# Kernel optimization log

Hardware: AMD Instinct MI355X
Metric: run time of the kernel (lower is better)

Reference implementation:

```python
import jax, jax.numpy as jnp
import numpy as np

K = 3  # reassembly kernel size (hardcoded in module)
S = 2  # upsample scale (hardcoded)
PAD = K // 2


def _nearest_up2(t):
    # F.interpolate(scale_factor=2, mode='nearest') on NCHW
    return jnp.repeat(jnp.repeat(t, 2, axis=2), 2, axis=3)


def _patches3x3(t):
    # F.unfold(kernel=3, pad=1) -> [B, C, 9, H, W], k = ki*3 + kj (row-major)
    B, C, H, W = t.shape
    tp = jnp.pad(t, ((0, 0), (0, 0), (PAD, PAD), (PAD, PAD)))
    return jnp.stack([tp[:, :, i:i + H, j:j + W] for i in range(K) for j in range(K)], axis=2)


def setup_inputs() -> dict:
    key = jax.random.key(0)
    k1, k2 = jax.random.split(key)
    x = jax.random.normal(k1, (2, 256, 128, 128), dtype=jnp.float32)
    W_off = jax.random.normal(k2, (2, 1, 5, 5), dtype=jnp.float32) * 1e-3  # normal_init std=0.001
    b_off = jnp.zeros((2,), dtype=jnp.float32)
    return {"x": x, "W_off": W_off, "b_off": b_off}


def reference(x, W_off, b_off):
    B, C, H, W = x.shape
    H2, W2 = S * H, S * W

    mean = jnp.mean(x, axis=1, keepdims=True)  # [B,1,H,W]

    # offset = tanh(conv5x5(nearest_up2(mean))) / 4 -> [B,2,2H,2W]
    mean_up = _nearest_up2(mean)
    off = jax.lax.conv_general_dilated(mean_up, W_off, (1, 1), ((2, 2), (2, 2)))
    offset = jnp.tanh(off + b_off[None, :, None, None]) / 4.0

    # center buffer: pixel_shuffle of [1,8,1,1]; per 2x2 cell, channel 0 varies with j, channel 1 with i
    cell = jnp.array([[[-0.25, 0.25], [-0.25, 0.25]],
                      [[-0.25, -0.25], [0.25, 0.25]]], dtype=x.dtype)  # [2(ch),2(i),2(j)]
    center = jnp.broadcast_to(cell[:, None, :, None, :], (2, H, 2, W, 2)).reshape(2, H2, W2)

    shift = center[None] + offset  # [B,2,2H,2W]

    # neighbor grid: n0 (fast, width) = [-1,0,1]*3 ; n1 (slow, height) = repeat([-1,0,1],3)
    n0 = jnp.tile(jnp.array([-1.0, 0.0, 1.0], dtype=x.dtype), 3)        # [9]
    n1 = jnp.repeat(jnp.array([-1.0, 0.0, 1.0], dtype=x.dtype), 3)      # [9]
    d2 = (shift[:, 0:1] - n0[None, :, None, None]) ** 2 + \
         (shift[:, 1:2] - n1[None, :, None, None]) ** 2                 # [B,9,2H,2W]
    kernels = 1.0 / (d2 + 0.2)

    # grad gating from 3x3 neighborhood of mean
    pm = _patches3x3(mean)[:, 0]            # [B,9,H,W]
    grad = pm - mean                        # broadcast over k
    grad = 1.0 / (grad ** 2 + 1.0)
    logits = _nearest_up2(grad) * kernels   # [B,9,2H,2W]
    kernels = jax.nn.softmax(logits, axis=1)

    # CARAFE: out[b,c,2h+p,2w+q] = sum_k kernels[b,k,2h+p,2w+q] * patches[b,c,k,h,w]
    patches = _patches3x3(x)                        # [B,C,9,H,W]
    Kr = kernels.reshape(B, K * K, H, S, W, S)      # [B,9,H,2,W,2]
    out = jnp.einsum('bkhpwq,bckhw->bchpwq', Kr, patches).reshape(B, C, H2, W2)
    return out
```

## Files before the change

### kernel.cpp

```cpp
#include <hip/hip_runtime.h>
#include <math.h>

#define B 2
#define C 256
#define H 128
#define W 128
#define H2 256
#define W2 256
#define CPT 16
#define TW 16

__global__ __launch_bounds__(1024) void mean_kernel(const float* __restrict__ x,
                                                    float* __restrict__ mean) {
    int bh = blockIdx.x;
    int b = bh / H, h = bh % H;
    int tid = threadIdx.x;
    int g  = tid >> 5;
    int w4 = tid & 31;

    const float4* xb = (const float4*)x + (size_t)b * C * (H * W / 4)
                       + (size_t)h * (W / 4) + w4;
    const size_t cstride = H * W / 4;

    float4 acc = make_float4(0.f, 0.f, 0.f, 0.f);
    #pragma unroll
    for (int i = 0; i < C / 32; ++i) {
        float4 v = xb[(size_t)(g * (C / 32) + i) * cstride];
        acc.x += v.x; acc.y += v.y; acc.z += v.z; acc.w += v.w;
    }

    __shared__ float4 sm[1024];
    sm[tid] = acc;
    __syncthreads();
    for (int s = 16; s >= 1; s >>= 1) {
        if (g < s) {
            float4 o = sm[tid + s * 32];
            acc.x += o.x; acc.y += o.y; acc.z += o.z; acc.w += o.w;
            sm[tid] = acc;
        }
        __syncthreads();
    }
    if (g == 0) {
        const float inv = 1.0f / C;
        float4 m = make_float4(acc.x * inv, acc.y * inv, acc.z * inv, acc.w * inv);
        ((float4*)mean)[(size_t)bh * (W / 4) + w4] = m;
    }
}

__global__ __launch_bounds__(256) void weights_kernel(const float* __restrict__ mean,
                                                      const float* __restrict__ Woff,
                                                      const float* __restrict__ boff,
                                                      float* __restrict__ Kw) {
    __shared__ float sm[10][12];
    __shared__ float sW[50];
    __shared__ float sb[2];

    int b  = blockIdx.z;
    int x0 = blockIdx.x * TW;
    int y0 = blockIdx.y * TW;
    int h0 = y0 >> 1, w0 = x0 >> 1;
    int tid = threadIdx.x;

    if (tid < 100) {
        int lh = tid / 10, lw = tid % 10;
        int hh = h0 - 1 + lh, ww = w0 - 1 + lw;
        sm[lh][lw] = (hh >= 0 && hh < H && ww >= 0 && ww < W)
                         ? mean[(size_t)b * H * W + hh * W + ww] : 0.f;
    }
    if (tid >= 128 && tid < 178) sW[tid - 128] = Woff[tid - 128];
    if (tid >= 192 && tid < 194) sb[tid - 192] = boff[tid - 192];
    __syncthreads();

    int tx = tid & 15, ty = tid >> 4;
    int y = y0 + ty, x = x0 + tx;

    float off0 = 0.f, off1 = 0.f;
    #pragma unroll
    for (int u = 0; u < 5; ++u) {
        int lh = ((y + u - 2) >> 1) - (h0 - 1);
        #pragma unroll
        for (int v = 0; v < 5; ++v) {
            int lw = ((x + v - 2) >> 1) - (w0 - 1);
            float m = sm[lh][lw];
            off0 += m * sW[u * 5 + v];
            off1 += m * sW[25 + u * 5 + v];
        }
    }
    float s0 = tanhf(off0 + sb[0]) * 0.25f + ((x & 1) ? 0.25f : -0.25f);
    float s1 = tanhf(off1 + sb[1]) * 0.25f + ((y & 1) ? 0.25f : -0.25f);

    int lhc = (ty >> 1) + 1;
    int lwc = (tx >> 1) + 1;
    float mc = sm[lhc][lwc];

    float lg[9];
    float mx = -1e30f;
    #pragma unroll
    for (int k = 0; k < 9; ++k) {
        int di = k / 3 - 1, dj = k % 3 - 1;
        float pm = sm[lhc + di][lwc + dj];
        float g = pm - mc;
        float grad = 1.0f / (g * g + 1.0f);
        float d0 = s0 - (float)dj;
        float d1 = s1 - (float)di;
        float kern = 1.0f / (d0 * d0 + d1 * d1 + 0.2f);
        float l = grad * kern;
        lg[k] = l;
        mx = fmaxf(mx, l);
    }
    float sum = 0.f;
    #pragma unroll
    for (int k = 0; k < 9; ++k) { lg[k] = expf(lg[k] - mx); sum += lg[k]; }
    float inv = 1.0f / sum;

    float* o = Kw + (size_t)b * 9 * (H2 * W2) + (size_t)y * W2 + x;
    #pragma unroll
    for (int k = 0; k < 9; ++k) o[(size_t)k * (H2 * W2)] = lg[k] * inv;
}

__global__ __launch_bounds__(256) void carafe_kernel(const float* __restrict__ x,
                                                     const float* __restrict__ Kw,
                                                     float* __restrict__ out) {
    int idx = blockIdx.x * blockDim.x + threadIdx.x;
    int w2 = idx & 63;
    int h  = (idx >> 6) & (H - 1);
    int cg = (idx >> 13) & (C / CPT - 1);
    int b  = idx >> 17;

    int w  = w2 * 2;
    int y0 = 2 * h, x0 = 2 * w;

    const float* kb = Kw + (size_t)b * 9 * (H2 * W2) + (size_t)y0 * W2 + x0;
    float4 wk[2][9];
    #pragma unroll
    for (int k = 0; k < 9; ++k) {
        wk[0][k] = *(const float4*)(kb + (size_t)k * (H2 * W2));
        wk[1][k] = *(const float4*)(kb + (size_t)k * (H2 * W2) + W2);
    }

    int off[3][4]; bool val[3][4];
    #pragma unroll
    for (int r = 0; r < 3; ++r) {
        int hh = h - 1 + r;
        #pragma unroll
        for (int c = 0; c < 4; ++c) {
            int ww = w - 1 + c;
            val[r][c] = (hh >= 0) & (hh < H) & (ww >= 0) & (ww < W);
            off[r][c] = hh * W + ww;
        }
    }

    const float* xb = x   + (size_t)(b * C + cg * CPT) * (H * W);
    float*       ob = out + (size_t)(b * C + cg * CPT) * (H2 * W2)
                          + (size_t)y0 * W2 + x0;

    #pragma unroll 2
    for (int cc = 0; cc < CPT; ++cc) {
        float p[3][4];
        #pragma unroll
        for (int r = 0; r < 3; ++r)
            #pragma unroll
            for (int c = 0; c < 4; ++c)
                p[r][c] = val[r][c] ? xb[off[r][c]] : 0.f;

        #pragma unroll
        for (int pp = 0; pp < 2; ++pp) {
            float4 acc = make_float4(0.f, 0.f, 0.f, 0.f);
            #pragma unroll
            for (int k = 0; k < 9; ++k) {
                int ki = k / 3, kj = k % 3;
                float a  = p[ki][kj];
                float bb = p[ki][kj + 1];
                acc.x += wk[pp][k].x * a;
                acc.y += wk[pp][k].y * a;
                acc.z += wk[pp][k].z * bb;
                acc.w += wk[pp][k].w * bb;
            }
            *(float4*)(ob + (size_t)pp * W2) = acc;
        }
        xb += H * W;
        ob += H2 * W2;
    }
}

extern "C" void kernel_launch(void* const* d_in, const int* in_sizes, int n_in,
                              void* d_out, int out_size, void* d_ws, size_t ws_size,
                              hipStream_t stream) {
    const float* x    = (const float*)d_in[0];
    const float* Woff = (const float*)d_in[1];
    const float* boff = (const float*)d_in[2];
    float* out = (float*)d_out;

    float* mean = (float*)d_ws;
    float* Kw   = mean + (size_t)B * H * W;

    mean_kernel<<<B * H, 1024, 0, stream>>>(x, mean);

    dim3 wgrid(W2 / TW, H2 / TW, B);
    weights_kernel<<<wgrid, 256, 0, stream>>>(mean, Woff, boff, Kw);

    int mt = B * (C / CPT) * H * (W / 2);
    carafe_kernel<<<mt / 256, 256, 0, stream>>>(x, Kw, out);
}
```

Baseline: 175.3 us.

## Fuse reassembly-weight computation into CARAFE kernel via shared-memory weight tile

Merges the weights kernel and the CARAFE kernel into one launch. Each block computes the softmax reassembly weights for a 16x16 output tile into shared memory, then reuses them across all 256 channels. This removes the global write and re-read of the 9-plane weight tensor and one kernel launch. In exchange the grid shrinks to 512 blocks, each thread handles 32 channels, and each warp covers a narrow 8-pixel-wide tile. That lowers parallelism and makes global loads and stores less coalesced.

```diff
diff --git a/kernel.cpp b/kernel.cpp
--- a/kernel.cpp
+++ b/kernel.cpp
@@ -7,8 +7,6 @@
 #define W 128
 #define H2 256
 #define W2 256
-#define CPT 16
-#define TW 16
 
 __global__ __launch_bounds__(1024) void mean_kernel(const float* __restrict__ x,
                                                     float* __restrict__ mean) {
@@ -47,18 +45,19 @@
     }
 }
 
-__global__ __launch_bounds__(256) void weights_kernel(const float* __restrict__ mean,
-                                                      const float* __restrict__ Woff,
-                                                      const float* __restrict__ boff,
-                                                      float* __restrict__ Kw) {
+__global__ __launch_bounds__(256) void fused_kernel(const float* __restrict__ x,
+                                                    const float* __restrict__ mean,
+                                                    const float* __restrict__ Woff,
+                                                    const float* __restrict__ boff,
+                                                    float* __restrict__ out) {
     __shared__ float sm[10][12];
     __shared__ float sW[50];
     __shared__ float sb[2];
+    __shared__ float sw[9][16][16];
 
     int b  = blockIdx.z;
-    int x0 = blockIdx.x * TW;
-    int y0 = blockIdx.y * TW;
-    int h0 = y0 >> 1, w0 = x0 >> 1;
+    int h0 = blockIdx.y * 8;
+    int w0 = blockIdx.x * 8;
     int tid = threadIdx.x;
 
     if (tid < 100) {
@@ -71,97 +70,90 @@
     if (tid >= 192 && tid < 194) sb[tid - 192] = boff[tid - 192];
     __syncthreads();
 
-    int tx = tid & 15, ty = tid >> 4;
-    int y = y0 + ty, x = x0 + tx;
+    {
+        int tx = tid & 15, ty = tid >> 4;
 
-    float off0 = 0.f, off1 = 0.f;
-    #pragma unroll
-    for (int u = 0; u < 5; ++u) {
-        int lh = ((y + u - 2) >> 1) - (h0 - 1);
+        float off0 = 0.f, off1 = 0.f;
         #pragma unroll
-        for (int v = 0; v < 5; ++v) {
-            int lw = ((x + v - 2) >> 1) - (w0 - 1);
-            float m = sm[lh][lw];
-            off0 += m * sW[u * 5 + v];
-            off1 += m * sW[25 + u * 5 + v];
+        for (int u = 0; u < 5; ++u) {
+            int lh = ((ty + u - 2) >> 1) + 1;
+            #pragma unroll
+            for (int v = 0; v < 5; ++v) {
+                int lw = ((tx + v - 2) >> 1) + 1;
+                float m = sm[lh][lw];
+                off0 += m * sW[u * 5 + v];
+                off1 += m * sW[25 + u * 5 + v];
+            }
         }
+        float s0 = tanhf(off0 + sb[0]) * 0.25f + ((tx & 1) ? 0.25f : -0.25f);
+        float s1 = tanhf(off1 + sb[1]) * 0.25f + ((ty & 1) ? 0.25f : -0.25f);
+
+        int lhc = (ty >> 1) + 1;
+        int lwc = (tx >> 1) + 1;
+        float mc = sm[lhc][lwc];
+
+        float lg[9];
+        float mx = -1e30f;
+        #pragma unroll
+        for (int k = 0; k < 9; ++k) {
+            int di = k / 3 - 1, dj = k % 3 - 1;
+            float pm = sm[lhc + di][lwc + dj];
+            float g = pm - mc;
+            float grad = 1.0f / (g * g + 1.0f);
+            float d0 = s0 - (float)dj;
+            float d1 = s1 - (float)di;
+            float kern = 1.0f / (d0 * d0 + d1 * d1 + 0.2f);
+            float l = grad * kern;
+            lg[k] = l;
+            mx = fmaxf(mx, l);
+        }
+        float sum = 0.f;
+        #pragma unroll
+        for (int k = 0; k < 9; ++k) { lg[k] = expf(lg[k] - mx); sum += lg[k]; }
+        float inv = 1.0f / sum;
+        #pragma unroll
+        for (int k = 0; k < 9; ++k) sw[k][ty][tx] = lg[k] * inv;
     }
-    float s0 = tanhf(off0 + sb[0]) * 0.25f + ((x & 1) ? 0.25f : -0.25f);
-    float s1 = tanhf(off1 + sb[1]) * 0.25f + ((y & 1) ? 0.25f : -0.25f);
+    __syncthreads();
 
-    int lhc = (ty >> 1) + 1;
-    int lwc = (tx >> 1) + 1;
-    float mc = sm[lhc][lwc];
+    int cp = tid & 3;
+    int r  = (tid >> 2) & 7;
+    int s  = tid >> 5;
 
-    float lg[9];
-    float mx = -1e30f;
-    #pragma unroll
-    for (int k = 0; k < 9; ++k) {
-        int di = k / 3 - 1, dj = k % 3 - 1;
-        float pm = sm[lhc + di][lwc + dj];
-        float g = pm - mc;
-        float grad = 1.0f / (g * g + 1.0f);
-        float d0 = s0 - (float)dj;
-        float d1 = s1 - (float)di;
-        float kern = 1.0f / (d0 * d0 + d1 * d1 + 0.2f);
-        float l = grad * kern;
-        lg[k] = l;
-        mx = fmaxf(mx, l);
-    }
-    float sum = 0.f;
-    #pragma unroll
-    for (int k = 0; k < 9; ++k) { lg[k] = expf(lg[k] - mx); sum += lg[k]; }
-    float inv = 1.0f / sum;
+    int h = h0 + r;
+    int w = w0 + 2 * cp;
 
-    float* o = Kw + (size_t)b * 9 * (H2 * W2) + (size_t)y * W2 + x;
-    #pragma unroll
-    for (int k = 0; k < 9; ++k) o[(size_t)k * (H2 * W2)] = lg[k] * inv;
-}
-
-__global__ __launch_bounds__(256) void carafe_kernel(const float* __restrict__ x,
-                                                     const float* __restrict__ Kw,
-                                                     float* __restrict__ out) {
-    int idx = blockIdx.x * blockDim.x + threadIdx.x;
-    int w2 = idx & 63;
-    int h  = (idx >> 6) & (H - 1);
-    int cg = (idx >> 13) & (C / CPT - 1);
-    int b  = idx >> 17;
-
-    int w  = w2 * 2;
-    int y0 = 2 * h, x0 = 2 * w;
-
-    const float* kb = Kw + (size_t)b * 9 * (H2 * W2) + (size_t)y0 * W2 + x0;
     float4 wk[2][9];
     #pragma unroll
     for (int k = 0; k < 9; ++k) {
-        wk[0][k] = *(const float4*)(kb + (size_t)k * (H2 * W2));
-        wk[1][k] = *(const float4*)(kb + (size_t)k * (H2 * W2) + W2);
+        wk[0][k] = *(const float4*)&sw[k][2 * r][4 * cp];
+        wk[1][k] = *(const float4*)&sw[k][2 * r + 1][4 * cp];
     }
 
     int off[3][4]; bool val[3][4];
     #pragma unroll
-    for (int r = 0; r < 3; ++r) {
-        int hh = h - 1 + r;
+    for (int rr = 0; rr < 3; ++rr) {
+        int hh = h - 1 + rr;
         #pragma unroll
-        for (int c = 0; c < 4; ++c) {
-            int ww = w - 1 + c;
-            val[r][c] = (hh >= 0) & (hh < H) & (ww >= 0) & (ww < W);
-            off[r][c] = hh * W + ww;
+        for (int cc = 0; cc < 4; ++cc) {
+            int ww = w - 1 + cc;
+            val[rr][cc] = (hh >= 0) & (hh < H) & (ww >= 0) & (ww < W);
+            off[rr][cc] = hh * W + ww;
         }
     }
 
-    const float* xb = x   + (size_t)(b * C + cg * CPT) * (H * W);
-    float*       ob = out + (size_t)(b * C + cg * CPT) * (H2 * W2)
-                          + (size_t)y0 * W2 + x0;
+    const float* xb = x   + (size_t)(b * C + s * 32) * (H * W);
+    float*       ob = out + (size_t)(b * C + s * 32) * (H2 * W2)
+                          + (size_t)(2 * h) * W2 + 2 * w;
 
     #pragma unroll 2
-    for (int cc = 0; cc < CPT; ++cc) {
+    for (int cc = 0; cc < 32; ++cc) {
         float p[3][4];
         #pragma unroll
-        for (int r = 0; r < 3; ++r)
+        for (int rr = 0; rr < 3; ++rr)
             #pragma unroll
-            for (int c = 0; c < 4; ++c)
-                p[r][c] = val[r][c] ? xb[off[r][c]] : 0.f;
+            for (int c2 = 0; c2 < 4; ++c2)
+                p[rr][c2] = val[rr][c2] ? xb[off[rr][c2]] : 0.f;
 
         #pragma unroll
         for (int pp = 0; pp < 2; ++pp) {
@@ -192,13 +184,9 @@
     float* out = (float*)d_out;
 
     float* mean = (float*)d_ws;
-    float* Kw   = mean + (size_t)B * H * W;
 
     mean_kernel<<<B * H, 1024, 0, stream>>>(x, mean);
 
-    dim3 wgrid(W2 / TW, H2 / TW, B);
-    weights_kernel<<<wgrid, 256, 0, stream>>>(mean, Woff, boff, Kw);
-
-    int mt = B * (C / CPT) * H * (W / 2);
-    carafe_kernel<<<mt / 256, 256, 0, stream>>>(x, Kw, out);
+    dim3 grid(W / 8, H / 8, B);
+    fused_kernel<<<grid, 256, 0, stream>>>(x, mean, Woff, boff, out);
 }
```

Result: slower. 230.2 us (+31.4%).
